# Performance work log

Measured on AMD Instinct MI355X. Metric: run time of the kernel, lower is better.

## Reference

```python
import jax, jax.numpy as jnp
import numpy as np

NEG_FILL = -10000.0  # matches masked_fill_(mask, -10000.0)


def setup_inputs() -> dict:
    key0 = jax.random.key(0)
    kq, kk, kv, km = jax.random.split(key0, 4)
    B, H, S, D = 2, 16, 2048, 64
    query = jax.random.normal(kq, (B, H, S, D), dtype=jnp.float32)
    key = jax.random.normal(kk, (B, H, S, D), dtype=jnp.float32)
    value = jax.random.normal(kv, (B, H, S, D), dtype=jnp.float32)
    # key-padding mask [B, S]; True = position is masked out
    mask = jax.random.randint(km, (B, S), 0, 2).astype(jnp.bool_)
    return {"query": query, "key": key, "value": value, "mask": mask}


def reference(query, key, value, mask):
    # scaled dot-product attention: [B,H,S,D] x [B,H,S,D] -> [B,H,S,S]
    scale = 1.0 / jnp.sqrt(jnp.asarray(query.shape[-1], query.dtype))
    scores = jnp.einsum('bhqd,bhkd->bhqk', query, key) * scale
    # mask [B,S] -> broadcast over heads and query positions as [B,1,1,S]
    scores = jnp.where(mask[:, None, None, :], jnp.asarray(NEG_FILL, scores.dtype), scores)
    attn = jax.nn.softmax(scores, axis=-1)
    # dropout probs are 0 (eval-mode identity)
    out = jnp.einsum('bhqk,bhkd->bhqd', attn, value)
    return out
```

## Files before the change

### kernel.cpp

```cpp
#include <hip/hip_runtime.h>
#include <hip/hip_bf16.h>
#include <stdint.h>

namespace {

constexpr int Bb = 2;
constexpr int Hh = 16;
constexpr int Ss = 2048;
constexpr int Dd = 64;
constexpr int KT = 64;
constexpr int NT = Ss / KT;
constexpr int TILE_BYTES = KT * Dd * 2;
constexpr int BH_BYTES = NT * TILE_BYTES;
constexpr size_t KPRE_BYTES = (size_t)Bb * Hh * Ss * Dd * 2;
constexpr size_t VPRE_OFF = KPRE_BYTES;
constexpr size_t MASK_OFF = 2 * KPRE_BYTES;

typedef __bf16 bf16x8 __attribute__((ext_vector_type(8)));
typedef float floatx4 __attribute__((ext_vector_type(4)));

typedef __attribute__((address_space(1))) const unsigned int guint;
typedef __attribute__((address_space(3))) unsigned int luint;

__device__ __forceinline__ void g2lds16(const void* g, void* l) {
  __builtin_amdgcn_global_load_lds((guint*)g, (luint*)l, 16, 0, 0);
}

__global__ __launch_bounds__(256) void preprocess4(
    const float* __restrict__ K, const float* __restrict__ V,
    const int* __restrict__ mask, uint8_t* __restrict__ ws)
{
  const int tid = threadIdx.x;
  const int kt = blockIdx.x;
  const int bh = blockIdx.y;

  if (blockIdx.z == 0) {
    const int c = tid & 7;
#pragma unroll
    for (int half = 0; half < 2; ++half) {
      const int row = (tid >> 3) + half * 32;
      const float4* src = (const float4*)(K + ((size_t)bh * 2048 + kt * 64 + row) * 64 + c * 8);
      const float4 a = src[0], b2 = src[1];
      bf16x8 pk;
      pk[0] = (__bf16)a.x;  pk[1] = (__bf16)a.y;  pk[2] = (__bf16)a.z;  pk[3] = (__bf16)a.w;
      pk[4] = (__bf16)b2.x; pk[5] = (__bf16)b2.y; pk[6] = (__bf16)b2.z; pk[7] = (__bf16)b2.w;
      uint8_t* dst = ws + (size_t)bh * BH_BYTES + kt * TILE_BYTES + row * 128 + ((c ^ (row & 7)) << 4);
      *(bf16x8*)dst = pk;
    }
    if (bh == 0 && kt < 16) {
      const int i = kt * 256 + tid;
      const int bb = i >> 11, key = i & 2047;
      const unsigned long long bal = __ballot(mask[bb * 2048 + key] != 0);
      if ((key & 63) == 0)
        ((unsigned long long*)(ws + MASK_OFF))[bb * NT + (key >> 6)] = bal;
    }
    return;
  }

  const int d2  = tid & 31;
  const int c16 = tid >> 5;
  const int s2 = c16 & 1, q = c16 >> 1;
  const int k0 = 32 * s2 + 4 * q;
  const float* vbase = V + ((size_t)bh * 2048 + kt * 64) * 64;
  float2 col[8];
#pragma unroll
  for (int j = 0; j < 4; ++j) {
    col[j]     = *(const float2*)(vbase + (size_t)(k0 + j) * 64 + 2 * d2);
    col[4 + j] = *(const float2*)(vbase + (size_t)(k0 + 16 + j) * 64 + 2 * d2);
  }
#pragma unroll
  for (int h = 0; h < 2; ++h) {
    const int d = 2 * d2 + h;
    bf16x8 pv;
#pragma unroll
    for (int j = 0; j < 4; ++j) {
      pv[j]     = (__bf16)(h ? col[j].y     : col[j].x);
      pv[4 + j] = (__bf16)(h ? col[4 + j].y : col[4 + j].x);
    }
    uint8_t* dst = ws + VPRE_OFF + (size_t)bh * BH_BYTES + kt * TILE_BYTES + d * 128 + ((c16 ^ (d & 7)) << 4);
    *(bf16x8*)dst = pv;
  }
}

#define NEGM (-14426.950408889634f)
#define MFMA16 __builtin_amdgcn_mfma_f32_16x16x32_bf16

__global__ __launch_bounds__(256, 2) void attn_fused11(
    const float* __restrict__ Q, const uint8_t* __restrict__ ws,
    float* __restrict__ Out)
{
  const int tid  = threadIdx.x;
  const int wave = tid >> 6;
  const int lane = tid & 63;
  const int ln   = lane & 15;
  const int quad = lane >> 4;

  const int bh   = blockIdx.x;
  const int qblk = blockIdx.y;
  const int b    = bh >> 4;

  const float* Qb = Q + (size_t)bh * Ss * Dd;
  float*       Ob = Out + (size_t)bh * Ss * Dd;
  const uint8_t* Kpre = ws + (size_t)bh * BH_BYTES;
  const uint8_t* Vpre = ws + VPRE_OFF + (size_t)bh * BH_BYTES;
  const unsigned long long* Mbits = (const unsigned long long*)(ws + MASK_OFF) + b * NT;

  __shared__ __align__(16) __bf16 Klds[3][64 * Dd];
  __shared__ __align__(16) __bf16 Vlds[3][64 * Dd];

  const int q0A = qblk * 128 + wave * 32;
  const int q0B = q0A + 16;

  const float QS = 0.125f * 1.44269504088896340736f;
  bf16x8 aqA0, aqA1, aqB0, aqB1;
  {
    const float* qpA = Qb + (size_t)(q0A + ln) * Dd + quad * 8;
    const float* qpB = Qb + (size_t)(q0B + ln) * Dd + quad * 8;
#pragma unroll
    for (int j = 0; j < 8; ++j) {
      aqA0[j] = (__bf16)(qpA[j] * QS);
      aqA1[j] = (__bf16)(qpA[32 + j] * QS);
      aqB0[j] = (__bf16)(qpB[j] * QS);
      aqB1[j] = (__bf16)(qpB[32 + j] * QS);
    }
  }

  floatx4 oA[4], oB[4];
  floatx4 laccA = (floatx4){0.f, 0.f, 0.f, 0.f};
  floatx4 laccB = (floatx4){0.f, 0.f, 0.f, 0.f};
#pragma unroll
  for (int nd = 0; nd < 4; ++nd) {
    oA[nd] = (floatx4){0.f, 0.f, 0.f, 0.f};
    oB[nd] = (floatx4){0.f, 0.f, 0.f, 0.f};
  }

  const int swz0 = (quad ^ (ln & 7)) << 4;
  const int swz1 = ((quad + 4) ^ (ln & 7)) << 4;
  const int soff = wave * 1024 + lane * 16;

  auto stage = [&](int it, __bf16* kl_, __bf16* vl_) {
    const uint8_t* kg = Kpre + it * TILE_BYTES;
    const uint8_t* vg = Vpre + it * TILE_BYTES;
    uint8_t* kl = (uint8_t*)kl_;
    uint8_t* vl = (uint8_t*)vl_;
    g2lds16(kg + soff,        kl + soff);
    g2lds16(kg + soff + 4096, kl + soff + 4096);
    g2lds16(vg + soff,        vl + soff);
    g2lds16(vg + soff + 4096, vl + soff + 4096);
  };

#define SPHASE(KB, MB, BPA, BPB)                                              \
  {                                                                           \
    const uint8_t* Kb_ = (const uint8_t*)(KB);                                \
    _Pragma("unroll")                                                         \
    for (int p = 0; p < 2; ++p) {                                             \
      const uint8_t* kr0 = Kb_ + ((2 * p) * 16 + ln) * 128;                   \
      const uint8_t* kr1 = Kb_ + ((2 * p + 1) * 16 + ln) * 128;               \
      const bf16x8 k00 = *(const bf16x8*)(kr0 + swz0);                        \
      const bf16x8 k10 = *(const bf16x8*)(kr0 + swz1);                        \
      const bf16x8 k01 = *(const bf16x8*)(kr1 + swz0);                        \
      const bf16x8 k11 = *(const bf16x8*)(kr1 + swz1);                        \
      const uint32_t bits0 = (uint32_t)((MB) >> ((2 * p) * 16 + quad * 4));   \
      const uint32_t bits1 = (uint32_t)((MB) >> ((2 * p + 1) * 16 + quad * 4));\
      floatx4 sA0, sA1, sB0, sB1;                                             \
      _Pragma("unroll")                                                       \
      for (int r = 0; r < 4; ++r) {                                           \
        const float b0v = ((bits0 >> r) & 1) ? NEGM : 0.f;                    \
        const float b1v = ((bits1 >> r) & 1) ? NEGM : 0.f;                    \
        sA0[r] = b0v; sB0[r] = b0v;                                           \
        sA1[r] = b1v; sB1[r] = b1v;                                           \
      }                                                                       \
      sA0 = MFMA16(k00, aqA0, sA0, 0, 0, 0);                                  \
      sA0 = MFMA16(k10, aqA1, sA0, 0, 0, 0);                                  \
      sB0 = MFMA16(k00, aqB0, sB0, 0, 0, 0);                                  \
      sB0 = MFMA16(k10, aqB1, sB0, 0, 0, 0);                                  \
      sA1 = MFMA16(k01, aqA0, sA1, 0, 0, 0);                                  \
      sA1 = MFMA16(k11, aqA1, sA1, 0, 0, 0);                                  \
      sB1 = MFMA16(k01, aqB0, sB1, 0, 0, 0);                                  \
      sB1 = MFMA16(k11, aqB1, sB1, 0, 0, 0);                                  \
      _Pragma("unroll")                                                       \
      for (int r = 0; r < 4; ++r) {                                           \
        const float pA0 = __builtin_amdgcn_exp2f(sA0[r]);                     \
        const float pA1 = __builtin_amdgcn_exp2f(sA1[r]);                     \
        const float pB0 = __builtin_amdgcn_exp2f(sB0[r]);                     \
        const float pB1 = __builtin_amdgcn_exp2f(sB1[r]);                     \
        laccA[r] += pA0 + pA1;                                                \
        laccB[r] += pB0 + pB1;                                                \
        BPA[p][r] = (__bf16)pA0; BPA[p][4 + r] = (__bf16)pA1;                 \
        BPB[p][r] = (__bf16)pB0; BPB[p][4 + r] = (__bf16)pB1;                 \
      }                                                                       \
    }                                                                         \
  }

#define PVPHASE(VB, BPA, BPB)                                                 \
  {                                                                           \
    const uint8_t* Vb_ = (const uint8_t*)(VB);                                \
    _Pragma("unroll")                                                         \
    for (int p = 0; p < 2; ++p) {                                             \
      _Pragma("unroll")                                                       \
      for (int nd = 0; nd < 4; ++nd) {                                        \
        const uint8_t* vrow = Vb_ + (nd * 16 + ln) * 128;                     \
        const bf16x8 w =                                                      \
            *(const bf16x8*)(vrow + (((quad * 2 + p) ^ (ln & 7)) << 4));      \
        oA[nd] = MFMA16(w, BPA[p], oA[nd], 0, 0, 0);                          \
        oB[nd] = MFMA16(w, BPB[p], oB[nd], 0, 0, 0);                          \
      }                                                                       \
    }                                                                         \
  }

#define BODY(IT, PBA, PBB, CBA, CBB)                                          \
  {                                                                           \
    __syncthreads();                                                          \
    if ((IT) + 1 < NT) stage((IT) + 1, knext, vnext);                         \
    const unsigned long long mb_ = Mbits[(IT)];                               \
    __builtin_amdgcn_s_setprio(1);                                            \
    SPHASE(kcur, mb_, CBA, CBB);                                              \
    PVPHASE(vprev, PBA, PBB);                                                 \
    __builtin_amdgcn_s_setprio(0);                                            \
    __bf16* t_;                                                               \
    t_ = kprev; kprev = kcur; kcur = knext; knext = t_;                       \
    t_ = vprev; vprev = vcur; vcur = vnext; vnext = t_;                       \
  }

  __bf16 *kprev = Klds[0], *kcur = Klds[1], *knext = Klds[2];
  __bf16 *vprev = Vlds[0], *vcur = Vlds[1], *vnext = Vlds[2];

  bf16x8 bpA0[2], bpB0[2], bpA1[2], bpB1[2];

  stage(0, kprev, vprev);
  __syncthreads();
  stage(1, kcur, vcur);
  {
    const unsigned long long mb_ = Mbits[0];
    __builtin_amdgcn_s_setprio(1);
    SPHASE(kprev, mb_, bpA0, bpB0);
    __builtin_amdgcn_s_setprio(0);
  }

  for (int it = 1; it < 31; it += 2) {
    BODY(it,     bpA0, bpB0, bpA1, bpB1);
    BODY(it + 1, bpA1, bpB1, bpA0, bpB0);
  }
  BODY(31, bpA0, bpB0, bpA1, bpB1);
  __builtin_amdgcn_s_setprio(1);
  PVPHASE(vprev, bpA1, bpB1);
  __builtin_amdgcn_s_setprio(0);

#undef BODY
#undef PVPHASE
#undef SPHASE

  float lA = (laccA[0] + laccA[1]) + (laccA[2] + laccA[3]);
  float lB = (laccB[0] + laccB[1]) + (laccB[2] + laccB[3]);
  lA += __shfl_xor(lA, 16); lA += __shfl_xor(lA, 32);
  lB += __shfl_xor(lB, 16); lB += __shfl_xor(lB, 32);
  const float iA = 1.0f / lA, iB = 1.0f / lB;
#pragma unroll
  for (int nd = 0; nd < 4; ++nd) {
    float4 wv;
    wv.x = oA[nd][0] * iA; wv.y = oA[nd][1] * iA;
    wv.z = oA[nd][2] * iA; wv.w = oA[nd][3] * iA;
    *(float4*)(Ob + (size_t)(q0A + ln) * Dd + nd * 16 + quad * 4) = wv;
    wv.x = oB[nd][0] * iB; wv.y = oB[nd][1] * iB;
    wv.z = oB[nd][2] * iB; wv.w = oB[nd][3] * iB;
    *(float4*)(Ob + (size_t)(q0B + ln) * Dd + nd * 16 + quad * 4) = wv;
  }
}

}

extern "C" void kernel_launch(void* const* d_in, const int* in_sizes, int n_in,
                              void* d_out, int out_size, void* d_ws, size_t ws_size,
                              hipStream_t stream) {
  const float* Q   = (const float*)d_in[0];
  const float* K   = (const float*)d_in[1];
  const float* V   = (const float*)d_in[2];
  const int*  mask = (const int*)d_in[3];
  float* Out = (float*)d_out;

  preprocess4<<<dim3(32, 32, 2), 256, 0, stream>>>(K, V, mask, (uint8_t*)d_ws);
  attn_fused11<<<dim3(Bb * Hh, Ss / 128), 256, 0, stream>>>(Q, (const uint8_t*)d_ws, Out);
  (void)ws_size; (void)in_sizes; (void)n_in; (void)out_size;
}
```

Measured before the change: 139.6 us.

## Stage 128-key tiles through registers with double-buffered LDS and fused PV

```diff
diff --git a/kernel.cpp b/kernel.cpp
--- a/kernel.cpp
+++ b/kernel.cpp
@@ -15,16 +15,11 @@
 constexpr size_t KPRE_BYTES = (size_t)Bb * Hh * Ss * Dd * 2;
 constexpr size_t VPRE_OFF = KPRE_BYTES;
 constexpr size_t MASK_OFF = 2 * KPRE_BYTES;
+constexpr int NIT = 16;
+constexpr int IT_BYTES = 2 * TILE_BYTES;
 
 typedef __bf16 bf16x8 __attribute__((ext_vector_type(8)));
 typedef float floatx4 __attribute__((ext_vector_type(4)));
-
-typedef __attribute__((address_space(1))) const unsigned int guint;
-typedef __attribute__((address_space(3))) unsigned int luint;
-
-__device__ __forceinline__ void g2lds16(const void* g, void* l) {
-  __builtin_amdgcn_global_load_lds((guint*)g, (luint*)l, 16, 0, 0);
-}
 
 __global__ __launch_bounds__(256) void preprocess4(
     const float* __restrict__ K, const float* __restrict__ V,
@@ -85,7 +80,7 @@
 #define NEGM (-14426.950408889634f)
 #define MFMA16 __builtin_amdgcn_mfma_f32_16x16x32_bf16
 
-__global__ __launch_bounds__(256, 2) void attn_fused11(
+__global__ __launch_bounds__(256, 2) void attn_fused13(
     const float* __restrict__ Q, const uint8_t* __restrict__ ws,
     float* __restrict__ Out)
 {
@@ -105,8 +100,8 @@
   const uint8_t* Vpre = ws + VPRE_OFF + (size_t)bh * BH_BYTES;
   const unsigned long long* Mbits = (const unsigned long long*)(ws + MASK_OFF) + b * NT;
 
-  __shared__ __align__(16) __bf16 Klds[3][64 * Dd];
-  __shared__ __align__(16) __bf16 Vlds[3][64 * Dd];
+  __shared__ __align__(16) __bf16 Klds[2][128 * Dd];
+  __shared__ __align__(16) __bf16 Vlds[2][128 * Dd];
 
   const int q0A = qblk * 128 + wave * 32;
   const int q0B = q0A + 16;
@@ -136,32 +131,63 @@
 
   const int swz0 = (quad ^ (ln & 7)) << 4;
   const int swz1 = ((quad + 4) ^ (ln & 7)) << 4;
-  const int soff = wave * 1024 + lane * 16;
-
-  auto stage = [&](int it, __bf16* kl_, __bf16* vl_) {
-    const uint8_t* kg = Kpre + it * TILE_BYTES;
-    const uint8_t* vg = Vpre + it * TILE_BYTES;
-    uint8_t* kl = (uint8_t*)kl_;
-    uint8_t* vl = (uint8_t*)vl_;
-    g2lds16(kg + soff,        kl + soff);
-    g2lds16(kg + soff + 4096, kl + soff + 4096);
-    g2lds16(vg + soff,        vl + soff);
-    g2lds16(vg + soff + 4096, vl + soff + 4096);
+  const int soff = wave * 4096 + lane * 16;
+
+  float4 ka[4], va[4], kb[4], vb[4];
+  auto loadRegs = [&](int it, float4* k, float4* v) {
+#pragma unroll
+    for (int i = 0; i < 4; ++i) {
+      k[i] = *(const float4*)(Kpre + (size_t)it * IT_BYTES + soff + i * 1024);
+      v[i] = *(const float4*)(Vpre + (size_t)it * IT_BYTES + soff + i * 1024);
+    }
   };
-
-#define SPHASE(KB, MB, BPA, BPB)                                              \
+  auto writeLds = [&](int buf, const float4* k, const float4* v) {
+#pragma unroll
+    for (int i = 0; i < 4; ++i) {
+      *(float4*)((uint8_t*)Klds[buf] + soff + i * 1024) = k[i];
+      *(float4*)((uint8_t*)Vlds[buf] + soff + i * 1024) = v[i];
+    }
+  };
+
+#define COMPUTE(CUR, MB0, MB1)                                                \
   {                                                                           \
-    const uint8_t* Kb_ = (const uint8_t*)(KB);                                \
+    const unsigned long long mb0 = (MB0);                                     \
+    const unsigned long long mb1 = (MB1);                                     \
+    const uint8_t* Kb = (const uint8_t*)Klds[(CUR)];                          \
+    const uint8_t* Vb = (const uint8_t*)Vlds[(CUR)];                          \
+    auto loadK = [&](int sub, bf16x8& b0, bf16x8& b1) {                       \
+      const uint8_t* krow =                                                   \
+          Kb + (sub >> 2) * 8192 + ((sub & 3) * 16 + ln) * 128;               \
+      b0 = *(const bf16x8*)(krow + swz0);                                     \
+      b1 = *(const bf16x8*)(krow + swz1);                                     \
+    };                                                                        \
+    auto loadV = [&](int p_, bf16x8* w) {                                     \
+      const int T = p_ >> 1, s2 = p_ & 1;                                     \
+      _Pragma("unroll")                                                       \
+      for (int nd = 0; nd < 4; ++nd) {                                        \
+        const uint8_t* vrow = Vb + T * 8192 + (nd * 16 + ln) * 128;           \
+        w[nd] = *(const bf16x8*)(vrow + (((quad * 2 + s2) ^ (ln & 7)) << 4)); \
+      }                                                                       \
+    };                                                                        \
+    __builtin_amdgcn_s_setprio(1);                                            \
+    bf16x8 kf0[2][2], kf1[2][2];                                              \
+    bf16x8 vf[2][4];                                                          \
+    loadK(0, kf0[0][0], kf1[0][0]);                                           \
+    loadK(1, kf0[0][1], kf1[0][1]);                                           \
+    loadV(0, vf[0]);                                                          \
     _Pragma("unroll")                                                         \
-    for (int p = 0; p < 2; ++p) {                                             \
-      const uint8_t* kr0 = Kb_ + ((2 * p) * 16 + ln) * 128;                   \
-      const uint8_t* kr1 = Kb_ + ((2 * p + 1) * 16 + ln) * 128;               \
-      const bf16x8 k00 = *(const bf16x8*)(kr0 + swz0);                        \
-      const bf16x8 k10 = *(const bf16x8*)(kr0 + swz1);                        \
-      const bf16x8 k01 = *(const bf16x8*)(kr1 + swz0);                        \
-      const bf16x8 k11 = *(const bf16x8*)(kr1 + swz1);                        \
-      const uint32_t bits0 = (uint32_t)((MB) >> ((2 * p) * 16 + quad * 4));   \
-      const uint32_t bits1 = (uint32_t)((MB) >> ((2 * p + 1) * 16 + quad * 4));\
+    for (int p = 0; p < 4; ++p) {                                             \
+      const int cb = p & 1, nb = cb ^ 1;                                      \
+      if (p < 3) {                                                            \
+        loadK(2 * p + 2, kf0[nb][0], kf1[nb][0]);                             \
+        loadK(2 * p + 3, kf0[nb][1], kf1[nb][1]);                             \
+        loadV(p + 1, vf[nb]);                                                 \
+      }                                                                       \
+      const unsigned long long mbx = (p & 2) ? mb1 : mb0;                     \
+      const uint32_t bits0 =                                                  \
+          (uint32_t)(mbx >> ((((2 * p) & 3) * 16) + quad * 4));               \
+      const uint32_t bits1 =                                                  \
+          (uint32_t)(mbx >> ((((2 * p + 1) & 3) * 16) + quad * 4));           \
       floatx4 sA0, sA1, sB0, sB1;                                             \
       _Pragma("unroll")                                                       \
       for (int r = 0; r < 4; ++r) {                                           \
@@ -170,14 +196,15 @@
         sA0[r] = b0v; sB0[r] = b0v;                                           \
         sA1[r] = b1v; sB1[r] = b1v;                                           \
       }                                                                       \
-      sA0 = MFMA16(k00, aqA0, sA0, 0, 0, 0);                                  \
-      sA0 = MFMA16(k10, aqA1, sA0, 0, 0, 0);                                  \
-      sB0 = MFMA16(k00, aqB0, sB0, 0, 0, 0);                                  \
-      sB0 = MFMA16(k10, aqB1, sB0, 0, 0, 0);                                  \
-      sA1 = MFMA16(k01, aqA0, sA1, 0, 0, 0);                                  \
-      sA1 = MFMA16(k11, aqA1, sA1, 0, 0, 0);                                  \
-      sB1 = MFMA16(k01, aqB0, sB1, 0, 0, 0);                                  \
-      sB1 = MFMA16(k11, aqB1, sB1, 0, 0, 0);                                  \
+      sA0 = MFMA16(kf0[cb][0], aqA0, sA0, 0, 0, 0);                           \
+      sA0 = MFMA16(kf1[cb][0], aqA1, sA0, 0, 0, 0);                           \
+      sB0 = MFMA16(kf0[cb][0], aqB0, sB0, 0, 0, 0);                           \
+      sB0 = MFMA16(kf1[cb][0], aqB1, sB0, 0, 0, 0);                           \
+      sA1 = MFMA16(kf0[cb][1], aqA0, sA1, 0, 0, 0);                           \
+      sA1 = MFMA16(kf1[cb][1], aqA1, sA1, 0, 0, 0);                           \
+      sB1 = MFMA16(kf0[cb][1], aqB0, sB1, 0, 0, 0);                           \
+      sB1 = MFMA16(kf1[cb][1], aqB1, sB1, 0, 0, 0);                           \
+      bf16x8 bpA, bpB;                                                        \
       _Pragma("unroll")                                                       \
       for (int r = 0; r < 4; ++r) {                                           \
         const float pA0 = __builtin_amdgcn_exp2f(sA0[r]);                     \
@@ -186,69 +213,37 @@
         const float pB1 = __builtin_amdgcn_exp2f(sB1[r]);                     \
         laccA[r] += pA0 + pA1;                                                \
         laccB[r] += pB0 + pB1;                                                \
-        BPA[p][r] = (__bf16)pA0; BPA[p][4 + r] = (__bf16)pA1;                 \
-        BPB[p][r] = (__bf16)pB0; BPB[p][4 + r] = (__bf16)pB1;                 \
+        bpA[r] = (__bf16)pA0; bpA[4 + r] = (__bf16)pA1;                       \
+        bpB[r] = (__bf16)pB0; bpB[4 + r] = (__bf16)pB1;                       \
+      }                                                                       \
+      _Pragma("unroll")                                                       \
+      for (int nd = 0; nd < 4; ++nd) {                                        \
+        oA[nd] = MFMA16(vf[cb][nd], bpA, oA[nd], 0, 0, 0);                    \
+        oB[nd] = MFMA16(vf[cb][nd], bpB, oB[nd], 0, 0, 0);                    \
       }                                                                       \
     }                                                                         \
-  }
-
-#define PVPHASE(VB, BPA, BPB)                                                 \
-  {                                                                           \
-    const uint8_t* Vb_ = (const uint8_t*)(VB);                                \
-    _Pragma("unroll")                                                         \
-    for (int p = 0; p < 2; ++p) {                                             \
-      _Pragma("unroll")                                                       \
-      for (int nd = 0; nd < 4; ++nd) {                                        \
-        const uint8_t* vrow = Vb_ + (nd * 16 + ln) * 128;                     \
-        const bf16x8 w =                                                      \
-            *(const bf16x8*)(vrow + (((quad * 2 + p) ^ (ln & 7)) << 4));      \
-        oA[nd] = MFMA16(w, BPA[p], oA[nd], 0, 0, 0);                          \
-        oB[nd] = MFMA16(w, BPB[p], oB[nd], 0, 0, 0);                          \
-      }                                                                       \
-    }                                                                         \
-  }
-
-#define BODY(IT, PBA, PBB, CBA, CBB)                                          \
+    __builtin_amdgcn_s_setprio(0);                                            \
+  }
+
+#define ITER(IT, WK, WV, LK, LV)                                              \
   {                                                                           \
     __syncthreads();                                                          \
-    if ((IT) + 1 < NT) stage((IT) + 1, knext, vnext);                         \
-    const unsigned long long mb_ = Mbits[(IT)];                               \
-    __builtin_amdgcn_s_setprio(1);                                            \
-    SPHASE(kcur, mb_, CBA, CBB);                                              \
-    PVPHASE(vprev, PBA, PBB);                                                 \
-    __builtin_amdgcn_s_setprio(0);                                            \
-    __bf16* t_;                                                               \
-    t_ = kprev; kprev = kcur; kcur = knext; knext = t_;                       \
-    t_ = vprev; vprev = vcur; vcur = vnext; vnext = t_;                       \
-  }
-
-  __bf16 *kprev = Klds[0], *kcur = Klds[1], *knext = Klds[2];
-  __bf16 *vprev = Vlds[0], *vcur = Vlds[1], *vnext = Vlds[2];
-
-  bf16x8 bpA0[2], bpB0[2], bpA1[2], bpB1[2];
-
-  stage(0, kprev, vprev);
-  __syncthreads();
-  stage(1, kcur, vcur);
-  {
-    const unsigned long long mb_ = Mbits[0];
-    __builtin_amdgcn_s_setprio(1);
-    SPHASE(kprev, mb_, bpA0, bpB0);
-    __builtin_amdgcn_s_setprio(0);
-  }
-
-  for (int it = 1; it < 31; it += 2) {
-    BODY(it,     bpA0, bpB0, bpA1, bpB1);
-    BODY(it + 1, bpA1, bpB1, bpA0, bpB0);
-  }
-  BODY(31, bpA0, bpB0, bpA1, bpB1);
-  __builtin_amdgcn_s_setprio(1);
-  PVPHASE(vprev, bpA1, bpB1);
-  __builtin_amdgcn_s_setprio(0);
-
-#undef BODY
-#undef PVPHASE
-#undef SPHASE
+    if ((IT) + 1 < NIT) writeLds(((IT) + 1) & 1, WK, WV);                     \
+    if ((IT) + 2 < NIT) loadRegs((IT) + 2, LK, LV);                           \
+    COMPUTE((IT) & 1, Mbits[2 * (IT)], Mbits[2 * (IT) + 1]);                  \
+  }
+
+  loadRegs(0, kb, vb);
+  writeLds(0, kb, vb);
+  loadRegs(1, ka, va);
+
+  for (int it2 = 0; it2 < NIT; it2 += 2) {
+    ITER(it2,     ka, va, kb, vb);
+    ITER(it2 + 1, kb, vb, ka, va);
+  }
+
+#undef ITER
+#undef COMPUTE
 
   float lA = (laccA[0] + laccA[1]) + (laccA[2] + laccA[3]);
   float lB = (laccB[0] + laccB[1]) + (laccB[2] + laccB[3]);
@@ -279,6 +274,6 @@
   float* Out = (float*)d_out;
 
   preprocess4<<<dim3(32, 32, 2), 256, 0, stream>>>(K, V, mask, (uint8_t*)d_ws);
-  attn_fused11<<<dim3(Bb * Hh, Ss / 128), 256, 0, stream>>>(Q, (const uint8_t*)d_ws, Out);
+  attn_fused13<<<dim3(Bb * Hh, Ss / 128), 256, 0, stream>>>(Q, (const uint8_t*)d_ws, Out);
   (void)ws_size; (void)in_sizes; (void)n_in; (void)out_size;
 }
```

Result: slower. 193.8 us (+38.8%).
